# Performance work log

Measured on AMD Instinct MI355X. Metric: run time of the kernel, lower is better.

The kernel has to match this reference:

```python
import jax, jax.numpy as jnp
import numpy as np

HEADS = 8
DIM_HEAD = 64
QUERY_DIM = 512
INNER_DIM = HEADS * DIM_HEAD  # 512


def setup_inputs() -> dict:
    key = jax.random.key(0)
    ks = jax.random.split(key, 6)
    B, S = 2, 4096
    hidden_states = jax.random.normal(ks[0], (B, S, QUERY_DIM), dtype=jnp.float32)
    # torch nn.Linear stores weight as [out, in]; y = x @ W.T (+ b)
    std = 0.02
    Wq = jax.random.normal(ks[1], (INNER_DIM, QUERY_DIM), dtype=jnp.float32) * std
    Wk = jax.random.normal(ks[2], (INNER_DIM, QUERY_DIM), dtype=jnp.float32) * std
    Wv = jax.random.normal(ks[3], (INNER_DIM, QUERY_DIM), dtype=jnp.float32) * std
    Wo = jax.random.normal(ks[4], (QUERY_DIM, INNER_DIM), dtype=jnp.float32) * std
    bo = jax.random.normal(ks[5], (QUERY_DIM,), dtype=jnp.float32) * std
    return {"hidden_states": hidden_states, "Wq": Wq, "Wk": Wk, "Wv": Wv, "Wo": Wo, "bo": bo}


def reference(hidden_states, Wq, Wk, Wv, Wo, bo):
    B, S, D = hidden_states.shape
    H, dh = HEADS, DIM_HEAD
    # QKV projections (no bias, per bias=False)
    q = jnp.einsum("bsd,ed->bse", hidden_states, Wq)
    k = jnp.einsum("bsd,ed->bse", hidden_states, Wk)
    v = jnp.einsum("bsd,ed->bse", hidden_states, Wv)
    # split heads: [B, S, H*dh] -> [B, H, S, dh]
    q = q.reshape(B, S, H, dh).transpose(0, 2, 1, 3)
    k = k.reshape(B, S, H, dh).transpose(0, 2, 1, 3)
    v = v.reshape(B, S, H, dh).transpose(0, 2, 1, 3)
    scale = 1.0 / jnp.sqrt(jnp.asarray(dh, dtype=q.dtype))
    scores = jnp.einsum("bhqd,bhkd->bhqk", q, k) * scale
    attn = jax.nn.softmax(scores, axis=-1)
    out = jnp.einsum("bhqk,bhkd->bhqd", attn, v)
    # merge heads back: [B, H, S, dh] -> [B, S, H*dh]
    out = out.transpose(0, 2, 1, 3).reshape(B, S, H * dh)
    # output projection (Linear with bias); dropout p=0.0 is identity
    return jnp.einsum("bse,de->bsd", out, Wo) + bo
```

## Files before the change

### kernel.cpp

```cpp
#include <hip/hip_runtime.h>
#include <stdint.h>

typedef _Float16 half_t;
typedef _Float16 half8 __attribute__((ext_vector_type(8)));
typedef __fp16 fp16x2 __attribute__((ext_vector_type(2)));
typedef float floatx4 __attribute__((ext_vector_type(4)));
typedef float floatx16 __attribute__((ext_vector_type(16)));
typedef unsigned int uint;
typedef unsigned int uint4v __attribute__((ext_vector_type(4)));

#define LOG2E 1.4426950408889634f

__device__ __forceinline__ void gload_lds16(const void* g, void* l) {
  __builtin_amdgcn_global_load_lds(
      (__attribute__((address_space(1))) void*)(uintptr_t)g,
      (__attribute__((address_space(3))) void*)(uintptr_t)l, 16, 0, 0);
}

__device__ __forceinline__ int swz64(int b)  { return b ^ (((b >> 7) & 3) << 4); }
__device__ __forceinline__ int swz128(int b) { return b ^ (((b >> 7) & 7) << 4); }

__device__ __forceinline__ uint pkrtz(float a, float b) {
  union { fp16x2 h; uint u; } cv;
  cv.h = __builtin_amdgcn_cvt_pkrtz(a, b);
  return cv.u;
}
__device__ __forceinline__ void pl32swap(uint &x, uint &y) {
  asm("v_permlane32_swap_b32 %0, %1" : "+v"(x), "+v"(y));
}
__device__ __forceinline__ half8 as_h8(uint4v v) {
  union { uint4v u; half8 h; } c; c.u = v; return c.h;
}

#define WAITB(N)                                          \
  asm volatile("s_waitcnt vmcnt(" #N ")" ::: "memory");   \
  __builtin_amdgcn_s_barrier();                           \
  __builtin_amdgcn_sched_barrier(0);

__global__ void cvt_x_kernel(const float* __restrict__ X, half_t* __restrict__ X16) {
  int i = (blockIdx.x * 256 + threadIdx.x) * 8;
  float4 u = *(const float4*)(X + i);
  float4 v = *(const float4*)(X + i + 4);
  half8 o = {(half_t)u.x, (half_t)u.y, (half_t)u.z, (half_t)u.w,
             (half_t)v.x, (half_t)v.y, (half_t)v.z, (half_t)v.w};
  *(half8*)(X16 + i) = o;
}

__global__ void cvt_w_kernel(const float* __restrict__ Wq, const float* __restrict__ Wk,
                             const float* __restrict__ Wv, const float* __restrict__ Wo,
                             half_t* __restrict__ W16) {
  int i = blockIdx.x * 256 + threadIdx.x;
  int widx = i >> 15;
  int j = (i & 32767) * 8;
  const float* src = (widx == 0) ? Wq : (widx == 1) ? Wk : (widx == 2) ? Wv : Wo;
  float sc = (widx == 0) ? 0.125f * LOG2E : 1.0f;
  float4 u = *(const float4*)(src + j);
  float4 v = *(const float4*)(src + j + 4);
  half8 o = {(half_t)(u.x * sc), (half_t)(u.y * sc), (half_t)(u.z * sc), (half_t)(u.w * sc),
             (half_t)(v.x * sc), (half_t)(v.y * sc), (half_t)(v.z * sc), (half_t)(v.w * sc)};
  *(half8*)(W16 + widx * 262144 + j) = o;
}

template <int MODE>
__global__ __launch_bounds__(256) void gemm_nt(
    const half_t* __restrict__ A, const half_t* __restrict__ B0,
    const half_t* __restrict__ B1, half_t* __restrict__ outh,
    half_t* __restrict__ outh2, float* __restrict__ outf,
    const float* __restrict__ bias) {
  __shared__ __attribute__((aligned(16))) half_t As[128 * 32];
  __shared__ __attribute__((aligned(16))) half_t Bs[128 * 32];

  const int tid = threadIdx.x;
  const int w = tid >> 6, l = tid & 63, g = l >> 4, c = l & 15;
  const int wr = w >> 1, wc = w & 1;
  const int bidx = blockIdx.x;

  int rt, ct;
  const half_t *Ab, *Bb;
  if (MODE == 0) {
    rt = bidx >> 3; ct = bidx & 7;
    Ab = A + (size_t)rt * 128 * 512;
    Bb = ((ct < 4) ? B0 : B1) + (size_t)(ct & 3) * 128 * 512;
  } else if (MODE == 1) {
    rt = bidx >> 6; ct = bidx & 63;
    Ab = A + (size_t)rt * 128 * 512;
    Bb = B0 + (size_t)ct * 128 * 512;
  } else {
    rt = bidx >> 2; ct = bidx & 3;
    Ab = A + (size_t)rt * 128 * 512;
    Bb = B0 + (size_t)ct * 128 * 512;
  }

  const floatx4 fzero = {0.f, 0.f, 0.f, 0.f};
  floatx4 acc[4][4];
#pragma unroll
  for (int m = 0; m < 4; ++m)
#pragma unroll
    for (int n = 0; n < 4; ++n) acc[m][n] = fzero;

  for (int kt = 0; kt < 16; ++kt) {
    __syncthreads();
#pragma unroll
    for (int i = 0; i < 2; ++i) {
      int rel = i * 4096 + tid * 16;
      int lg = swz64(rel);
      int row = lg >> 6, inner = (lg & 63) >> 1;
      gload_lds16(Ab + (size_t)row * 512 + kt * 32 + inner, As + (rel >> 1));
      gload_lds16(Bb + (size_t)row * 512 + kt * 32 + inner, Bs + (rel >> 1));
    }
    __syncthreads();
    half8 a[4], b[4];
#pragma unroll
    for (int m = 0; m < 4; ++m)
      a[m] = *(const half8*)&As[swz64(((wr * 64 + m * 16 + c) << 6) + (g << 4)) >> 1];
#pragma unroll
    for (int n = 0; n < 4; ++n)
      b[n] = *(const half8*)&Bs[swz64(((wc * 64 + n * 16 + c) << 6) + (g << 4)) >> 1];
#pragma unroll
    for (int m = 0; m < 4; ++m)
#pragma unroll
      for (int n = 0; n < 4; ++n)
        acc[m][n] = __builtin_amdgcn_mfma_f32_16x16x32_f16(a[m], b[n], acc[m][n], 0, 0, 0);
  }

  const int r0 = wr * 64, c0 = wc * 64;
  if (MODE == 0) {
    half_t* O = ((ct < 4) ? outh : outh2) + (size_t)rt * 128 * 512 + (size_t)(ct & 3) * 128;
#pragma unroll
    for (int m = 0; m < 4; ++m)
#pragma unroll
      for (int j = 0; j < 4; ++j)
#pragma unroll
        for (int n = 0; n < 4; ++n)
          O[(size_t)(r0 + m * 16 + g * 4 + j) * 512 + c0 + n * 16 + c] = (half_t)acc[m][n][j];
  } else if (MODE == 1) {
    half_t* O = outh + (size_t)(ct >> 5) * 2097152 + (size_t)(ct & 31) * 128;
#pragma unroll
    for (int m = 0; m < 4; ++m)
#pragma unroll
      for (int j = 0; j < 4; ++j)
#pragma unroll
        for (int n = 0; n < 4; ++n)
          O[(size_t)(rt * 128 + r0 + m * 16 + g * 4 + j) * 4096 + c0 + n * 16 + c] =
              (half_t)acc[m][n][j];
  } else {
    float* O = outf + (size_t)rt * 128 * 512 + ct * 128;
    float bv[4];
#pragma unroll
    for (int n = 0; n < 4; ++n) bv[n] = bias[ct * 128 + c0 + n * 16 + c];
#pragma unroll
    for (int m = 0; m < 4; ++m)
#pragma unroll
      for (int j = 0; j < 4; ++j)
#pragma unroll
        for (int n = 0; n < 4; ++n)
          O[(size_t)(r0 + m * 16 + g * 4 + j) * 512 + c0 + n * 16 + c] = acc[m][n][j] + bv[n];
  }
}

__global__ __launch_bounds__(256, 2) void attn_kernel(
    const half_t* __restrict__ Q16, const half_t* __restrict__ K16,
    const half_t* __restrict__ Vt, half_t* __restrict__ O16) {
  __shared__ __attribute__((aligned(16))) char smem[81920];
  half_t* kb_lds = (half_t*)smem;
  half_t* vb_lds = (half_t*)(smem + 40960);

  const int tid = threadIdx.x;
  const int w = tid >> 6, l = tid & 63, lo = l & 31, h = l >> 5;
  const int kw = w >> 1, qw = w & 1;
  const int bid = (blockIdx.x & 7) * 64 + (blockIdx.x >> 3);
  const int bh = bid >> 5, qt = bid & 31;
  const int b = bh >> 3, hh = bh & 7;

  const half_t* Qb = Q16 + (size_t)(b * 4096 + qt * 128 + qw * 64) * 512 + hh * 64;
  const half_t* Kb = K16 + (size_t)b * 4096 * 512 + hh * 64;
  const half_t* Vb = Vt + (size_t)bh * 262144;
  half_t* Ob = O16 + (size_t)(b * 4096 + qt * 128 + qw * 64) * 512 + hh * 64;

  half8 qa[2][4];
#pragma unroll
  for (int qm = 0; qm < 2; ++qm)
#pragma unroll
    for (int ks = 0; ks < 4; ++ks)
      qa[qm][ks] = *(const half8*)(Qb + (size_t)(qm * 32 + lo) * 512 + ks * 16 + h * 8);

  floatx16 acc[2][2];
#pragma unroll
  for (int qm = 0; qm < 2; ++qm)
#pragma unroll
    for (int dn = 0; dn < 2; ++dn)
#pragma unroll
      for (int r = 0; r < 16; ++r) acc[qm][dn][r] = 0.f;
  float lf[2] = {0.f, 0.f};

  floatx16 fz16;
#pragma unroll
  for (int r = 0; r < 16; ++r) fz16[r] = 0.f;

  auto stage = [&](int slot, int t) {
#pragma unroll
    for (int i = 0; i < 2; ++i) {
      int rel = i * 4096 + tid * 16;
      int lg = swz128(rel);
      int row = lg >> 7, inner = (lg & 127) >> 1;
      gload_lds16(Kb + (size_t)(t * 64 + row) * 512 + inner,
                  kb_lds + slot * 4096 + (rel >> 1));
      gload_lds16(Vb + (size_t)row * 4096 + t * 64 + inner,
                  vb_lds + slot * 4096 + (rel >> 1));
    }
  };

  auto qk_only = [&](int slotQK, floatx16 (&sNew)[2]) {
    const half_t* kt = kb_lds + slotQK * 4096;
#pragma unroll
    for (int ks = 0; ks < 4; ++ks) {
      int byte = ((kw * 32 + lo) << 7) + (ks << 5) + (h << 4);
      half8 ka = *(const half8*)&kt[swz128(byte) >> 1];
      if (ks == 0) {
        sNew[0] = __builtin_amdgcn_mfma_f32_32x32x16_f16(ka, qa[0][0], fz16, 0, 0, 0);
        sNew[1] = __builtin_amdgcn_mfma_f32_32x32x16_f16(ka, qa[1][0], fz16, 0, 0, 0);
      } else {
        sNew[0] = __builtin_amdgcn_mfma_f32_32x32x16_f16(ka, qa[0][ks], sNew[0], 0, 0, 0);
        sNew[1] = __builtin_amdgcn_mfma_f32_32x32x16_f16(ka, qa[1][ks], sNew[1], 0, 0, 0);
      }
    }
  };

  auto chunk = [&](floatx16 (&sOld)[2], int qm, int ksb, uint4v (&pa)[2][2]) {
    float e[8];
    float ps = 0.f;
#pragma unroll
    for (int j = 0; j < 8; ++j) {
      e[j] = __builtin_amdgcn_exp2f(sOld[qm][8 * ksb + j]);
      ps += e[j];
    }
    lf[qm] += ps;
    uint x0 = pkrtz(e[0], e[1]), x1 = pkrtz(e[2], e[3]);
    uint y0 = pkrtz(e[4], e[5]), y1 = pkrtz(e[6], e[7]);
    pl32swap(x0, y0);
    pl32swap(x1, y1);
    pa[qm][ksb] = (uint4v){x0, x1, y0, y1};
  };

  auto pv = [&](int slotPV, uint4v (&pa)[2][2]) {
    const half_t* vt = vb_lds + slotPV * 4096;
    __builtin_amdgcn_s_setprio(1);
#pragma unroll
    for (int dn = 0; dn < 2; ++dn)
#pragma unroll
      for (int ks = 0; ks < 2; ++ks) {
        int byte = ((dn * 32 + lo) << 7) + ((kw * 32 + ks * 16 + h * 8) << 1);
        half8 vb = *(const half8*)&vt[swz128(byte) >> 1];
#pragma unroll
        for (int qm = 0; qm < 2; ++qm)
          acc[qm][dn] =
              __builtin_amdgcn_mfma_f32_32x32x16_f16(as_h8(pa[qm][ks]), vb, acc[qm][dn], 0, 0, 0);
      }
    __builtin_amdgcn_s_setprio(0);
  };

  auto full_round = [&](int slotQK, int slotPV, floatx16 (&sOld)[2], floatx16 (&sNew)[2]) {
    const half_t* kt = kb_lds + slotQK * 4096;
    uint4v pa[2][2];
#pragma unroll
    for (int ks = 0; ks < 4; ++ks) {
      int byte = ((kw * 32 + lo) << 7) + (ks << 5) + (h << 4);
      half8 ka = *(const half8*)&kt[swz128(byte) >> 1];
      if (ks == 0) {
        sNew[0] = __builtin_amdgcn_mfma_f32_32x32x16_f16(ka, qa[0][0], fz16, 0, 0, 0);
        sNew[1] = __builtin_amdgcn_mfma_f32_32x32x16_f16(ka, qa[1][0], fz16, 0, 0, 0);
      } else {
        sNew[0] = __builtin_amdgcn_mfma_f32_32x32x16_f16(ka, qa[0][ks], sNew[0], 0, 0, 0);
        sNew[1] = __builtin_amdgcn_mfma_f32_32x32x16_f16(ka, qa[1][ks], sNew[1], 0, 0, 0);
      }
      chunk(sOld, ks >> 1, ks & 1, pa);
    }
    pv(slotPV, pa);
  };

  floatx16 sA[2], sB[2];

  stage(0, 0);
  stage(1, 1);
  stage(2, 2);

  WAITB(8)
  stage(3, 3);
  qk_only(0, sA);

  int sStage = 4, sQK = 1, sPV = 0;
  for (int r = 1; r <= 60; r += 2) {
    WAITB(8)
    stage(sStage, r + 3);
    full_round(sQK, sPV, sA, sB);
    sStage = (sStage == 4) ? 0 : sStage + 1;
    sQK = (sQK == 4) ? 0 : sQK + 1;
    sPV = (sPV == 4) ? 0 : sPV + 1;

    WAITB(8)
    stage(sStage, r + 4);
    full_round(sQK, sPV, sB, sA);
    sStage = (sStage == 4) ? 0 : sStage + 1;
    sQK = (sQK == 4) ? 0 : sQK + 1;
    sPV = (sPV == 4) ? 0 : sPV + 1;
  }
  WAITB(8)
  full_round(sQK, sPV, sA, sB);
  sQK = (sQK == 4) ? 0 : sQK + 1;
  sPV = (sPV == 4) ? 0 : sPV + 1;
  WAITB(4)
  full_round(sQK, sPV, sB, sA);
  sQK = (sQK == 4) ? 0 : sQK + 1;
  sPV = (sPV == 4) ? 0 : sPV + 1;
  WAITB(0)
  full_round(sQK, sPV, sA, sB);
  sPV = (sPV == 4) ? 0 : sPV + 1;

  {
    uint4v pa[2][2];
#pragma unroll
    for (int ks = 0; ks < 4; ++ks) chunk(sB, ks >> 1, ks & 1, pa);
    pv(sPV, pa);
  }

#pragma unroll
  for (int qm = 0; qm < 2; ++qm) lf[qm] += __shfl_xor(lf[qm], 32);

  float* red = (float*)smem;
  float* redl = (float*)(smem + 32768);

  __syncthreads();
  if (kw == 1) {
#pragma unroll
    for (int qm = 0; qm < 2; ++qm) {
      redl[(qw * 2 + qm) * 64 + l] = lf[qm];
#pragma unroll
      for (int dn = 0; dn < 2; ++dn)
#pragma unroll
        for (int r = 0; r < 16; ++r)
          red[((((qw * 2 + qm) * 2 + dn) * 16) + r) * 64 + l] = acc[qm][dn][r];
    }
  }
  __syncthreads();
  if (kw == 0) {
    float inv[2];
#pragma unroll
    for (int qm = 0; qm < 2; ++qm)
      inv[qm] = 1.0f / (lf[qm] + redl[(qw * 2 + qm) * 64 + l]);
#pragma unroll
    for (int qm = 0; qm < 2; ++qm)
#pragma unroll
      for (int r = 0; r < 16; ++r) {
        int ro = (r & 3) + 8 * (r >> 2) + 4 * h;
        float iv = __shfl(inv[qm], ro);
#pragma unroll
        for (int dn = 0; dn < 2; ++dn) {
          float o = (acc[qm][dn][r] + red[((((qw * 2 + qm) * 2 + dn) * 16) + r) * 64 + l]) * iv;
          Ob[(size_t)(qm * 32 + ro) * 512 + dn * 32 + lo] = (half_t)o;
        }
      }
  }
}

extern "C" void kernel_launch(void* const* d_in, const int* in_sizes, int n_in,
                              void* d_out, int out_size, void* d_ws, size_t ws_size,
                              hipStream_t stream) {
  const float* X  = (const float*)d_in[0];
  const float* Wq = (const float*)d_in[1];
  const float* Wk = (const float*)d_in[2];
  const float* Wv = (const float*)d_in[3];
  const float* Wo = (const float*)d_in[4];
  const float* bo = (const float*)d_in[5];
  float* out = (float*)d_out;

  char* ws = (char*)d_ws;
  half_t* X16  = (half_t*)(ws);
  half_t* W16  = (half_t*)(ws + 8388608);
  half_t* Q16  = (half_t*)(ws + 10485760);
  half_t* K16  = (half_t*)(ws + 18874368);
  half_t* VtW  = (half_t*)(ws + 27262976);
  half_t* O16  = (half_t*)(ws + 35651584);
  half_t* Wq16 = W16;
  half_t* Wk16 = W16 + 262144;
  half_t* Wv16 = W16 + 524288;
  half_t* Wo16 = W16 + 786432;

  cvt_x_kernel<<<2048, 256, 0, stream>>>(X, X16);
  cvt_w_kernel<<<512, 256, 0, stream>>>(Wq, Wk, Wv, Wo, W16);
  gemm_nt<0><<<512, 256, 0, stream>>>(X16, Wq16, Wk16, Q16, K16, nullptr, nullptr);
  gemm_nt<1><<<256, 256, 0, stream>>>(Wv16, X16, nullptr, VtW, nullptr, nullptr, nullptr);
  attn_kernel<<<512, 256, 0, stream>>>(Q16, K16, VtW, O16);
  gemm_nt<2><<<256, 256, 0, stream>>>(O16, Wo16, nullptr, nullptr, nullptr, out, bo);
}
```

Before: 134.2 us.

## Multi-stage LDS pipeline in projection GEMMs and merge conversion kernels

```diff
diff --git a/kernel.cpp b/kernel.cpp
--- a/kernel.cpp
+++ b/kernel.cpp
@@ -37,28 +37,30 @@
   __builtin_amdgcn_s_barrier();                           \
   __builtin_amdgcn_sched_barrier(0);
 
-__global__ void cvt_x_kernel(const float* __restrict__ X, half_t* __restrict__ X16) {
-  int i = (blockIdx.x * 256 + threadIdx.x) * 8;
-  float4 u = *(const float4*)(X + i);
-  float4 v = *(const float4*)(X + i + 4);
-  half8 o = {(half_t)u.x, (half_t)u.y, (half_t)u.z, (half_t)u.w,
-             (half_t)v.x, (half_t)v.y, (half_t)v.z, (half_t)v.w};
-  *(half8*)(X16 + i) = o;
-}
-
-__global__ void cvt_w_kernel(const float* __restrict__ Wq, const float* __restrict__ Wk,
-                             const float* __restrict__ Wv, const float* __restrict__ Wo,
-                             half_t* __restrict__ W16) {
-  int i = blockIdx.x * 256 + threadIdx.x;
-  int widx = i >> 15;
-  int j = (i & 32767) * 8;
-  const float* src = (widx == 0) ? Wq : (widx == 1) ? Wk : (widx == 2) ? Wv : Wo;
-  float sc = (widx == 0) ? 0.125f * LOG2E : 1.0f;
-  float4 u = *(const float4*)(src + j);
-  float4 v = *(const float4*)(src + j + 4);
-  half8 o = {(half_t)(u.x * sc), (half_t)(u.y * sc), (half_t)(u.z * sc), (half_t)(u.w * sc),
-             (half_t)(v.x * sc), (half_t)(v.y * sc), (half_t)(v.z * sc), (half_t)(v.w * sc)};
-  *(half8*)(W16 + widx * 262144 + j) = o;
+__global__ void cvt_kernel(const float* __restrict__ X, const float* __restrict__ Wq,
+                           const float* __restrict__ Wk, const float* __restrict__ Wv,
+                           const float* __restrict__ Wo, half_t* __restrict__ X16,
+                           half_t* __restrict__ W16) {
+  int gid = blockIdx.x;
+  if (gid < 2048) {
+    int i = (gid * 256 + threadIdx.x) * 8;
+    float4 u = *(const float4*)(X + i);
+    float4 v = *(const float4*)(X + i + 4);
+    half8 o = {(half_t)u.x, (half_t)u.y, (half_t)u.z, (half_t)u.w,
+               (half_t)v.x, (half_t)v.y, (half_t)v.z, (half_t)v.w};
+    *(half8*)(X16 + i) = o;
+  } else {
+    int i = (gid - 2048) * 256 + threadIdx.x;
+    int widx = i >> 15;
+    int j = (i & 32767) * 8;
+    const float* src = (widx == 0) ? Wq : (widx == 1) ? Wk : (widx == 2) ? Wv : Wo;
+    float sc = (widx == 0) ? 0.125f * LOG2E : 1.0f;
+    float4 u = *(const float4*)(src + j);
+    float4 v = *(const float4*)(src + j + 4);
+    half8 o = {(half_t)(u.x * sc), (half_t)(u.y * sc), (half_t)(u.z * sc), (half_t)(u.w * sc),
+               (half_t)(v.x * sc), (half_t)(v.y * sc), (half_t)(v.z * sc), (half_t)(v.w * sc)};
+    *(half8*)(W16 + widx * 262144 + j) = o;
+  }
 }
 
 template <int MODE>
@@ -67,8 +69,8 @@
     const half_t* __restrict__ B1, half_t* __restrict__ outh,
     half_t* __restrict__ outh2, float* __restrict__ outf,
     const float* __restrict__ bias) {
-  __shared__ __attribute__((aligned(16))) half_t As[128 * 32];
-  __shared__ __attribute__((aligned(16))) half_t Bs[128 * 32];
+  __shared__ __attribute__((aligned(16))) half_t As[4][4096];
+  __shared__ __attribute__((aligned(16))) half_t Bs[4][4096];
 
   const int tid = threadIdx.x;
   const int w = tid >> 6, l = tid & 63, g = l >> 4, c = l & 15;
@@ -98,30 +100,47 @@
 #pragma unroll
     for (int n = 0; n < 4; ++n) acc[m][n] = fzero;
 
-  for (int kt = 0; kt < 16; ++kt) {
-    __syncthreads();
+  auto stage = [&](int slot, int kt) {
 #pragma unroll
     for (int i = 0; i < 2; ++i) {
       int rel = i * 4096 + tid * 16;
       int lg = swz64(rel);
       int row = lg >> 6, inner = (lg & 63) >> 1;
-      gload_lds16(Ab + (size_t)row * 512 + kt * 32 + inner, As + (rel >> 1));
-      gload_lds16(Bb + (size_t)row * 512 + kt * 32 + inner, Bs + (rel >> 1));
-    }
-    __syncthreads();
+      gload_lds16(Ab + (size_t)row * 512 + kt * 32 + inner, As[slot] + (rel >> 1));
+      gload_lds16(Bb + (size_t)row * 512 + kt * 32 + inner, Bs[slot] + (rel >> 1));
+    }
+  };
+
+  auto compute = [&](int slot) {
     half8 a[4], b[4];
 #pragma unroll
     for (int m = 0; m < 4; ++m)
-      a[m] = *(const half8*)&As[swz64(((wr * 64 + m * 16 + c) << 6) + (g << 4)) >> 1];
+      a[m] = *(const half8*)&As[slot][swz64(((wr * 64 + m * 16 + c) << 6) + (g << 4)) >> 1];
 #pragma unroll
     for (int n = 0; n < 4; ++n)
-      b[n] = *(const half8*)&Bs[swz64(((wc * 64 + n * 16 + c) << 6) + (g << 4)) >> 1];
+      b[n] = *(const half8*)&Bs[slot][swz64(((wc * 64 + n * 16 + c) << 6) + (g << 4)) >> 1];
 #pragma unroll
     for (int m = 0; m < 4; ++m)
 #pragma unroll
       for (int n = 0; n < 4; ++n)
         acc[m][n] = __builtin_amdgcn_mfma_f32_16x16x32_f16(a[m], b[n], acc[m][n], 0, 0, 0);
-  }
+  };
+
+  stage(0, 0);
+  stage(1, 1);
+  stage(2, 2);
+
+  for (int kt = 0; kt < 13; ++kt) {
+    WAITB(8)
+    stage((kt + 3) & 3, kt + 3);
+    compute(kt & 3);
+  }
+  WAITB(8)
+  compute(1);
+  WAITB(4)
+  compute(2);
+  WAITB(0)
+  compute(3);
 
   const int r0 = wr * 64, c0 = wc * 64;
   if (MODE == 0) {
@@ -385,8 +404,7 @@
   half_t* Wv16 = W16 + 524288;
   half_t* Wo16 = W16 + 786432;
 
-  cvt_x_kernel<<<2048, 256, 0, stream>>>(X, X16);
-  cvt_w_kernel<<<512, 256, 0, stream>>>(Wq, Wk, Wv, Wo, W16);
+  cvt_kernel<<<2560, 256, 0, stream>>>(X, Wq, Wk, Wv, Wo, X16, W16);
   gemm_nt<0><<<512, 256, 0, stream>>>(X16, Wq16, Wk16, Q16, K16, nullptr, nullptr);
   gemm_nt<1><<<256, 256, 0, stream>>>(Wv16, X16, nullptr, VtW, nullptr, nullptr, nullptr);
   attn_kernel<<<512, 256, 0, stream>>>(Q16, K16, VtW, O16);
```

New measurement: 122.1 us. 1.1x faster.
